# Kernel optimization log

Measured on AMD Instinct MI355X. Metric: run time of the kernel, lower is better.

## Reference

```python
import jax, jax.numpy as jnp
import numpy as np

B, CIN, COUT, SDIM, RES, K = 8, 512, 512, 512, 64, 3
AFF_SCALE = 1.0 / np.sqrt(SDIM)          # LinearAct: 1/sqrt(in_features)
CONV_SCALE = 1.0 / np.sqrt(CIN * K * K)  # ModulatedConv2d: 1/sqrt(in*k*k)
LRELU_GAIN = np.sqrt(2.0)                # bias_act 'lrelu' default gain


def setup_inputs() -> dict:
    key = jax.random.key(0)
    k = jax.random.split(key, 5)
    x = jax.random.normal(k[0], (B, CIN, RES, RES), dtype=jnp.float32)
    w = jax.random.normal(k[1], (B, SDIM), dtype=jnp.float32)
    noise = jax.random.normal(k[2], (B, 1, RES, RES), dtype=jnp.float32)
    affine_w = jax.random.normal(k[3], (CIN, SDIM), dtype=jnp.float32)
    affine_b = jnp.ones((CIN,), dtype=jnp.float32)          # bias.data.fill_(1.0)
    conv_w = jax.random.normal(k[4], (COUT, CIN, K, K), dtype=jnp.float32)
    noise_scale = jnp.asarray(0.1, dtype=jnp.float32)        # InjectNoise.scale (nonzero for a meaningful test)
    bias = jnp.zeros((COUT,), dtype=jnp.float32)
    return {"x": x, "w": w, "noise": noise, "affine_w": affine_w,
            "affine_b": affine_b, "conv_w": conv_w,
            "noise_scale": noise_scale, "bias": bias}


def reference(x, w, noise, affine_w, affine_b, conv_w, noise_scale, bias):
    # affine (LinearAct, act='linear'): style = w @ (W*scale)^T + b
    style = jnp.einsum('bs,cs->bc', w, affine_w * AFF_SCALE) + affine_b  # [B, CIN]

    # modulate + demodulate: per-sample weight [B, COUT, CIN, K, K]
    wt = conv_w[None] * style[:, None, :, None, None] * CONV_SCALE
    d = jax.lax.rsqrt(jnp.sum(wt * wt, axis=(2, 3, 4), keepdims=True) + 1e-8)
    wt = wt * d

    # grouped conv (groups=B) == per-sample conv; flip_weight=True -> plain correlation
    def conv_one(xi, wi):
        return jax.lax.conv_general_dilated(
            xi[None], wi, window_strides=(1, 1), padding=[(1, 1), (1, 1)],
            dimension_numbers=('NCHW', 'OIHW', 'NCHW'))[0]

    y = jax.vmap(conv_one)(x, wt)  # [B, COUT, RES, RES]

    # noise -> bias -> lrelu(0.2) * sqrt(2)
    y = y + noise * noise_scale
    y = jax.nn.leaky_relu(y + bias[None, :, None, None], 0.2) * LRELU_GAIN
    return y
```

## Files before the change

kernel.cpp:

```cpp
#include <hip/hip_runtime.h>
#include <hip/hip_bf16.h>

typedef unsigned short u16;

#define BATCH 8
#define CIN 512
#define COUT 512
#define SDIM 512
#define RES 64
#define PIX (RES * RES)
#define NKT 72

__device__ __constant__ static const float kAffScale  = 0.04419417382415922f;
__device__ __constant__ static const float kConvScale = 0.014731391274719742f;
__device__ __constant__ static const float kGain      = 1.4142135623730951f;

typedef __bf16 bf16x8 __attribute__((ext_vector_type(8)));
typedef float  f32x4  __attribute__((ext_vector_type(4)));

__global__ void style_k(const float* __restrict__ w, const float* __restrict__ aw,
                        const float* __restrict__ ab, float* __restrict__ style,
                        float* __restrict__ zbuf) {
  int tid = blockIdx.x * 256 + threadIdx.x;
  if (blockIdx.x == 0 && threadIdx.x < 64) zbuf[threadIdx.x] = 0.0f;
  int b = tid >> 9, c = tid & 511;
  const float* wp = w + b * SDIM;
  const float* ap = aw + c * SDIM;
  float s = 0.0f;
  for (int k = 0; k < SDIM; ++k) s += wp[k] * ap[k];
  style[tid] = s * kAffScale + ab[c];
}

__global__ void cw2_k(const float* __restrict__ cw, float* __restrict__ cw2) {
  int tid = blockIdx.x * 256 + threadIdx.x;
  const float* p = cw + tid * 9;
  float s = 0.0f;
  #pragma unroll
  for (int t = 0; t < 9; ++t) { float v = p[t]; s += v * v; }
  cw2[tid] = s;
}

__global__ void fac_k(const float* __restrict__ style, const float* __restrict__ cw2,
                      float* __restrict__ fac) {
  int wid  = blockIdx.x * 4 + (threadIdx.x >> 6);
  int lane = threadIdx.x & 63;
  int b = wid >> 9, o = wid & 511;
  const float* st = style + b * CIN;
  const float* c2 = cw2 + o * CIN;
  float s = 0.0f;
  for (int i = lane; i < CIN; i += 64) { float sv = st[i]; s += sv * sv * c2[i]; }
  #pragma unroll
  for (int off = 32; off; off >>= 1) s += __shfl_xor(s, off);
  if (lane == 0) {
    float d = rsqrtf(s * kConvScale * kConvScale + 1e-8f);
    fac[wid] = d * kConvScale;
  }
}

__global__ void wcast_k(const float* __restrict__ cw, u16* __restrict__ wbt) {
  int tid = blockIdx.x * 256 + threadIdx.x;
  int o = tid >> 9, i = tid & 511;
  const float* p = cw + tid * 9;
  #pragma unroll
  for (int t = 0; t < 9; ++t) {
    __hip_bfloat16 h = __float2bfloat16(p[t]);
    wbt[((size_t)(t * 16 + (i >> 5)) * 512 + o) * 32 + (i & 31)] = *(u16*)&h;
  }
}

__global__ void modx_k(const float* __restrict__ x, const float* __restrict__ style,
                       u16* __restrict__ xst) {
  __shared__ float t[64][65];
  int b  = blockIdx.z;
  int it = blockIdx.y * 64;
  int pt = blockIdx.x * 64;
  int tp = threadIdx.x & 63;
  int tr = threadIdx.x >> 6;
  for (int r = tr; r < 64; r += 4) {
    int i = it + r;
    t[r][tp] = x[(b * CIN + i) * PIX + pt + tp] * style[b * CIN + i];
  }
  __syncthreads();
  int i = it + tp;
  size_t base = ((size_t)(b * 16 + (i >> 5)) * PIX) * 32 + (i & 31);
  for (int r = tr; r < 64; r += 4) {
    __hip_bfloat16 h = __float2bfloat16(t[tp][r]);
    xst[base + (size_t)(pt + r) * 32] = *(u16*)&h;
  }
}

__launch_bounds__(512, 2)
__global__ void gemm_k(const u16* __restrict__ wbt, const u16* __restrict__ xst,
                       const float* __restrict__ fac, const float* __restrict__ noise,
                       const float* __restrict__ nscale_p, const float* __restrict__ bias,
                       const float* __restrict__ zbuf, float* __restrict__ y) {
  __shared__ __align__(16) u16 Abuf[2][16384];
  __shared__ __align__(16) u16 Bbuf[2][16384];

  const int tid = threadIdx.x;
  const int bid = blockIdx.x;
  const int swz = (bid & 7) * 32 + (bid >> 3);
  const int mt = swz >> 7;
  const int nt = swz & 127;
  const int b  = nt >> 4;
  const int pimg  = (nt & 15) * 256;
  const int hbase = pimg >> 6;

  const int lane = tid & 63;
  const int wv = tid >> 6;
  const int wm = wv >> 2;
  const int wn = wv & 3;
  const int l15 = lane & 15, l4 = lane >> 4;
  const int slot = (l4 ^ ((l15 >> 1) & 3)) * 8;

  const int sgE = ((tid & 3) ^ ((tid >> 3) & 3)) << 3;
  int aoff[2], boff[2], hr[2], wc[2];
  #pragma unroll
  for (int p = 0; p < 2; ++p) {
    int row = (p * 512 + tid) >> 2;
    aoff[p] = (mt * 256 + row) * 32 + sgE;
    boff[p] = (pimg + row) * 32 + sgE;
    hr[p] = hbase + (row >> 6);
    wc[p] = row & 63;
  }

  auto stA = [&](int ktx, int kh) {
    if (ktx >= NKT) ktx -= NKT;
    const int d = ktx & 1;
    const u16* pan = wbt + ((size_t)((ktx >> 3) * 16 + ((ktx & 7) << 1) + kh) << 14);
    #pragma unroll
    for (int p = 0; p < 2; ++p) {
      const u16* src = pan + aoff[p];
      __builtin_amdgcn_global_load_lds(
          (const __attribute__((address_space(1))) void*)src,
          (__attribute__((address_space(3))) void*)(&Abuf[d][kh * 8192 + (p * 512 + tid) * 8]),
          16, 0, 0);
    }
  };
  auto stB = [&](int ktx, int kh) {
    if (ktx >= NKT) ktx -= NKT;
    const int tap = ktx >> 3;
    const int dy  = tap < 3 ? -1 : (tap < 6 ? 0 : 1);
    const int dx  = (tap - (tap < 3 ? 0 : (tap < 6 ? 3 : 6))) - 1;
    const int d   = ktx & 1;
    const u16* pan = xst + ((size_t)(b * 16 + ((ktx & 7) << 1) + kh) << 17);
    const int shiftE = (dy * 64 + dx) * 32;
    #pragma unroll
    for (int p = 0; p < 2; ++p) {
      int hh = hr[p] + dy, ww = wc[p] + dx;
      const u16* src = ((unsigned)hh < 64u && (unsigned)ww < 64u)
          ? pan + (boff[p] + shiftE) : (const u16*)zbuf;
      __builtin_amdgcn_global_load_lds(
          (const __attribute__((address_space(1))) void*)src,
          (__attribute__((address_space(3))) void*)(&Bbuf[d][kh * 8192 + (p * 512 + tid) * 8]),
          16, 0, 0);
    }
  };

  f32x4 acc[8][4];
  #pragma unroll
  for (int i = 0; i < 8; ++i)
    #pragma unroll
    for (int j = 0; j < 4; ++j) acc[i][j] = (f32x4){0.f, 0.f, 0.f, 0.f};

  stA(0, 0); stB(0, 0); stA(0, 1); stB(0, 1); stA(1, 0); stB(1, 0);
  asm volatile("s_waitcnt vmcnt(8)" ::: "memory");
  __builtin_amdgcn_s_barrier();

#define LDA(mi, kh) (*(const bf16x8*)&Ab[(kh) * 8192 + (wm * 128 + (mi) * 16 + l15) * 32 + slot])
#define LDB(ni, kh) (*(const bf16x8*)&Bb[(kh) * 8192 + (wn * 64 + (ni) * 16 + l15) * 32 + slot])

  for (int kt = 0; kt < NKT; ++kt) {
    const u16* Ab = &Abuf[kt & 1][0];
    const u16* Bb = &Bbuf[kt & 1][0];
    bf16x8 bfr[4], af[4];

    #pragma unroll
    for (int ni = 0; ni < 4; ++ni) bfr[ni] = LDB(ni, 0);
    #pragma unroll
    for (int j = 0; j < 4; ++j) af[j] = LDA(j, 0);
    stA(kt + 1, 1);
    __builtin_amdgcn_s_barrier();
    __builtin_amdgcn_s_setprio(1);
    #pragma unroll
    for (int j = 0; j < 4; ++j)
      #pragma unroll
      for (int ni = 0; ni < 4; ++ni)
        acc[j][ni] = __builtin_amdgcn_mfma_f32_16x16x32_bf16(af[j], bfr[ni], acc[j][ni], 0, 0, 0);
    __builtin_amdgcn_s_setprio(0);
    __builtin_amdgcn_s_barrier();

    #pragma unroll
    for (int j = 0; j < 4; ++j) af[j] = LDA(4 + j, 0);
    stB(kt + 1, 1);
    __builtin_amdgcn_s_barrier();
    __builtin_amdgcn_s_setprio(1);
    #pragma unroll
    for (int j = 0; j < 4; ++j)
      #pragma unroll
      for (int ni = 0; ni < 4; ++ni)
        acc[4 + j][ni] = __builtin_amdgcn_mfma_f32_16x16x32_bf16(af[j], bfr[ni], acc[4 + j][ni], 0, 0, 0);
    __builtin_amdgcn_s_setprio(0);
    asm volatile("s_waitcnt vmcnt(8)" ::: "memory");
    __builtin_amdgcn_s_barrier();

    #pragma unroll
    for (int ni = 0; ni < 4; ++ni) bfr[ni] = LDB(ni, 1);
    #pragma unroll
    for (int j = 0; j < 4; ++j) af[j] = LDA(j, 1);
    stA(kt + 2, 0);
    __builtin_amdgcn_s_barrier();
    __builtin_amdgcn_s_setprio(1);
    #pragma unroll
    for (int j = 0; j < 4; ++j)
      #pragma unroll
      for (int ni = 0; ni < 4; ++ni)
        acc[j][ni] = __builtin_amdgcn_mfma_f32_16x16x32_bf16(af[j], bfr[ni], acc[j][ni], 0, 0, 0);
    __builtin_amdgcn_s_setprio(0);
    __builtin_amdgcn_s_barrier();

    #pragma unroll
    for (int j = 0; j < 4; ++j) af[j] = LDA(4 + j, 1);
    stB(kt + 2, 0);
    __builtin_amdgcn_s_barrier();
    __builtin_amdgcn_s_setprio(1);
    #pragma unroll
    for (int j = 0; j < 4; ++j)
      #pragma unroll
      for (int ni = 0; ni < 4; ++ni)
        acc[4 + j][ni] = __builtin_amdgcn_mfma_f32_16x16x32_bf16(af[j], bfr[ni], acc[4 + j][ni], 0, 0, 0);
    __builtin_amdgcn_s_setprio(0);
    asm volatile("s_waitcnt vmcnt(8)" ::: "memory");
    __builtin_amdgcn_s_barrier();
  }
#undef LDA
#undef LDB

  const float ns = nscale_p[0];
  float nz[4];
  #pragma unroll
  for (int ni = 0; ni < 4; ++ni) {
    int pix = pimg + wn * 64 + ni * 16 + l15;
    nz[ni] = noise[b * PIX + pix] * ns;
  }
  #pragma unroll
  for (int mi = 0; mi < 8; ++mi) {
    int o = mt * 256 + wm * 128 + mi * 16 + l4 * 4;
    f32x4 fv = *(const f32x4*)&fac[b * COUT + o];
    f32x4 bv = *(const f32x4*)&bias[o];
    #pragma unroll
    for (int r = 0; r < 4; ++r) {
      float* yp = y + (size_t)(b * COUT + o + r) * PIX + pimg + wn * 64 + l15;
      #pragma unroll
      for (int ni = 0; ni < 4; ++ni) {
        float v = acc[mi][ni][r] * fv[r] + nz[ni] + bv[r];
        v = (v > 0.0f ? v : 0.2f * v) * kGain;
        yp[ni * 16] = v;
      }
    }
  }
}

extern "C" void kernel_launch(void* const* d_in, const int* in_sizes, int n_in,
                              void* d_out, int out_size, void* d_ws, size_t ws_size,
                              hipStream_t stream) {
  const float* x      = (const float*)d_in[0];
  const float* w      = (const float*)d_in[1];
  const float* noise  = (const float*)d_in[2];
  const float* aff_w  = (const float*)d_in[3];
  const float* aff_b  = (const float*)d_in[4];
  const float* conv_w = (const float*)d_in[5];
  const float* nscale = (const float*)d_in[6];
  const float* bias   = (const float*)d_in[7];
  float* y = (float*)d_out;

  char* ws = (char*)d_ws;
  float* style = (float*)(ws);
  float* fac   = (float*)(ws + 16384);
  float* cw2   = (float*)(ws + 32768);
  float* zbuf  = (float*)(ws + 1081344);
  u16*   wbt   = (u16*)(ws + 1081600);
  u16*   xst   = (u16*)(ws + 5800192);

  style_k<<<16, 256, 0, stream>>>(w, aff_w, aff_b, style, zbuf);
  cw2_k<<<1024, 256, 0, stream>>>(conv_w, cw2);
  fac_k<<<1024, 256, 0, stream>>>(style, cw2, fac);
  wcast_k<<<1024, 256, 0, stream>>>(conv_w, wbt);
  modx_k<<<dim3(64, 8, 8), 256, 0, stream>>>(x, style, xst);
  gemm_k<<<256, 512, 0, stream>>>(wbt, xst, fac, noise, nscale, bias, zbuf, y);
}
```

Measured before the change: 231.6 us.

## Software-pipeline LDS fragment loads one phase ahead of MFMA in conv loop

Restructures the main GEMM loop so LDS reads for the next MFMA phase are issued before the current phase's MFMAs, using separate register sets (af03/af47, bfr0/bfr1) and prefetching the next k-tile's first fragments across the loop boundary. It replaces some barriers with finer lgkmcnt/vmcnt waits and sched_barriers so LDS latency overlaps tensor math. This costs extra VGPRs, which could reduce occupancy, and depends on the wait counts being exactly right for correctness.

Measured after the change: 217.1 us. 6.3% less time.

```diff
diff --git a/kernel.cpp b/kernel.cpp
--- a/kernel.cpp
+++ b/kernel.cpp
@@ -163,78 +163,93 @@
     #pragma unroll
     for (int j = 0; j < 4; ++j) acc[i][j] = (f32x4){0.f, 0.f, 0.f, 0.f};
 
+#define LDAp(base, mi, kh) (*(const bf16x8*)&(base)[(kh) * 8192 + (wm * 128 + (mi) * 16 + l15) * 32 + slot])
+#define LDBp(base, ni, kh) (*(const bf16x8*)&(base)[(kh) * 8192 + (wn * 64 + (ni) * 16 + l15) * 32 + slot])
+
   stA(0, 0); stB(0, 0); stA(0, 1); stB(0, 1); stA(1, 0); stB(1, 0);
   asm volatile("s_waitcnt vmcnt(8)" ::: "memory");
   __builtin_amdgcn_s_barrier();
 
-#define LDA(mi, kh) (*(const bf16x8*)&Ab[(kh) * 8192 + (wm * 128 + (mi) * 16 + l15) * 32 + slot])
-#define LDB(ni, kh) (*(const bf16x8*)&Bb[(kh) * 8192 + (wn * 64 + (ni) * 16 + l15) * 32 + slot])
+  bf16x8 af03[4], af47[4], bfr0[4], bfr1[4];
+  {
+    const u16* Ab = &Abuf[0][0];
+    const u16* Bb = &Bbuf[0][0];
+    #pragma unroll
+    for (int ni = 0; ni < 4; ++ni) bfr0[ni] = LDBp(Bb, ni, 0);
+    #pragma unroll
+    for (int j = 0; j < 4; ++j) af03[j] = LDAp(Ab, j, 0);
+  }
 
   for (int kt = 0; kt < NKT; ++kt) {
-    const u16* Ab = &Abuf[kt & 1][0];
-    const u16* Bb = &Bbuf[kt & 1][0];
-    bf16x8 bfr[4], af[4];
-
-    #pragma unroll
-    for (int ni = 0; ni < 4; ++ni) bfr[ni] = LDB(ni, 0);
-    #pragma unroll
-    for (int j = 0; j < 4; ++j) af[j] = LDA(j, 0);
+    const u16* Ab  = &Abuf[kt & 1][0];
+    const u16* Bb  = &Bbuf[kt & 1][0];
+    const u16* AbN = &Abuf[(kt + 1) & 1][0];
+    const u16* BbN = &Bbuf[(kt + 1) & 1][0];
+
+    #pragma unroll
+    for (int j = 0; j < 4; ++j) af47[j] = LDAp(Ab, 4 + j, 0);
     stA(kt + 1, 1);
+    asm volatile("s_waitcnt lgkmcnt(4)" ::: "memory");
+    __builtin_amdgcn_sched_barrier(0);
+    __builtin_amdgcn_s_setprio(1);
+    #pragma unroll
+    for (int j = 0; j < 4; ++j)
+      #pragma unroll
+      for (int ni = 0; ni < 4; ++ni)
+        acc[j][ni] = __builtin_amdgcn_mfma_f32_16x16x32_bf16(af03[j], bfr0[ni], acc[j][ni], 0, 0, 0);
+    __builtin_amdgcn_s_setprio(0);
+    asm volatile("s_waitcnt vmcnt(6)" ::: "memory");
     __builtin_amdgcn_s_barrier();
+
+    #pragma unroll
+    for (int ni = 0; ni < 4; ++ni) bfr1[ni] = LDBp(Bb, ni, 1);
+    #pragma unroll
+    for (int j = 0; j < 4; ++j) af03[j] = LDAp(Ab, j, 1);
+    stB(kt + 1, 1);
+    asm volatile("s_waitcnt lgkmcnt(8)" ::: "memory");
+    __builtin_amdgcn_sched_barrier(0);
     __builtin_amdgcn_s_setprio(1);
     #pragma unroll
     for (int j = 0; j < 4; ++j)
       #pragma unroll
       for (int ni = 0; ni < 4; ++ni)
-        acc[j][ni] = __builtin_amdgcn_mfma_f32_16x16x32_bf16(af[j], bfr[ni], acc[j][ni], 0, 0, 0);
+        acc[4 + j][ni] = __builtin_amdgcn_mfma_f32_16x16x32_bf16(af47[j], bfr0[ni], acc[4 + j][ni], 0, 0, 0);
     __builtin_amdgcn_s_setprio(0);
     __builtin_amdgcn_s_barrier();
 
     #pragma unroll
-    for (int j = 0; j < 4; ++j) af[j] = LDA(4 + j, 0);
-    stB(kt + 1, 1);
+    for (int j = 0; j < 4; ++j) af47[j] = LDAp(Ab, 4 + j, 1);
+    stA(kt + 2, 0);
+    asm volatile("s_waitcnt lgkmcnt(4)" ::: "memory");
+    __builtin_amdgcn_sched_barrier(0);
+    __builtin_amdgcn_s_setprio(1);
+    #pragma unroll
+    for (int j = 0; j < 4; ++j)
+      #pragma unroll
+      for (int ni = 0; ni < 4; ++ni)
+        acc[j][ni] = __builtin_amdgcn_mfma_f32_16x16x32_bf16(af03[j], bfr1[ni], acc[j][ni], 0, 0, 0);
+    __builtin_amdgcn_s_setprio(0);
+    asm volatile("s_waitcnt vmcnt(6)" ::: "memory");
     __builtin_amdgcn_s_barrier();
+
+    #pragma unroll
+    for (int ni = 0; ni < 4; ++ni) bfr0[ni] = LDBp(BbN, ni, 0);
+    #pragma unroll
+    for (int j = 0; j < 4; ++j) af03[j] = LDAp(AbN, j, 0);
+    stB(kt + 2, 0);
+    asm volatile("s_waitcnt lgkmcnt(8)" ::: "memory");
+    __builtin_amdgcn_sched_barrier(0);
     __builtin_amdgcn_s_setprio(1);
     #pragma unroll
     for (int j = 0; j < 4; ++j)
       #pragma unroll
       for (int ni = 0; ni < 4; ++ni)
-        acc[4 + j][ni] = __builtin_amdgcn_mfma_f32_16x16x32_bf16(af[j], bfr[ni], acc[4 + j][ni], 0, 0, 0);
-    __builtin_amdgcn_s_setprio(0);
-    asm volatile("s_waitcnt vmcnt(8)" ::: "memory");
-    __builtin_amdgcn_s_barrier();
-
-    #pragma unroll
-    for (int ni = 0; ni < 4; ++ni) bfr[ni] = LDB(ni, 1);
-    #pragma unroll
-    for (int j = 0; j < 4; ++j) af[j] = LDA(j, 1);
-    stA(kt + 2, 0);
-    __builtin_amdgcn_s_barrier();
-    __builtin_amdgcn_s_setprio(1);
-    #pragma unroll
-    for (int j = 0; j < 4; ++j)
-      #pragma unroll
-      for (int ni = 0; ni < 4; ++ni)
-        acc[j][ni] = __builtin_amdgcn_mfma_f32_16x16x32_bf16(af[j], bfr[ni], acc[j][ni], 0, 0, 0);
+        acc[4 + j][ni] = __builtin_amdgcn_mfma_f32_16x16x32_bf16(af47[j], bfr1[ni], acc[4 + j][ni], 0, 0, 0);
     __builtin_amdgcn_s_setprio(0);
     __builtin_amdgcn_s_barrier();
-
-    #pragma unroll
-    for (int j = 0; j < 4; ++j) af[j] = LDA(4 + j, 1);
-    stB(kt + 2, 0);
-    __builtin_amdgcn_s_barrier();
-    __builtin_amdgcn_s_setprio(1);
-    #pragma unroll
-    for (int j = 0; j < 4; ++j)
-      #pragma unroll
-      for (int ni = 0; ni < 4; ++ni)
-        acc[4 + j][ni] = __builtin_amdgcn_mfma_f32_16x16x32_bf16(af[j], bfr[ni], acc[4 + j][ni], 0, 0, 0);
-    __builtin_amdgcn_s_setprio(0);
-    asm volatile("s_waitcnt vmcnt(8)" ::: "memory");
-    __builtin_amdgcn_s_barrier();
-  }
-#undef LDA
-#undef LDB
+  }
+#undef LDAp
+#undef LDBp
 
   const float ns = nscale_p[0];
   float nz[4];
```

## Store activations in zero-padded 66x66 panels and unroll GEMM loop by two

Applied to the files above, without the earlier changes.

Activations are now written into per-channel-group panels with a one-pixel zero border (66x66), filled by a new border-zeroing kernel. This removes the per-load bounds checks and the zbuf redirection in the conv GEMM's B-tile loads. The main loop is unrolled by two so LDS buffer indices are compile-time constants, and explicit lgkmcnt waits plus sched_barriers are added before each MFMA block. The cost is an extra small kernel launch and slightly larger workspace, and the explicit waits may limit the compiler's ability to overlap LDS reads with MFMAs.

New measurement: 204.3 us. -11.8%, faster.

```diff
diff --git a/kernel.cpp b/kernel.cpp
--- a/kernel.cpp
+++ b/kernel.cpp
@@ -10,6 +10,8 @@
 #define RES 64
 #define PIX (RES * RES)
 #define NKT 72
+#define PPIX 4356
+#define PANEL_E 139392
 
 __device__ __constant__ static const float kAffScale  = 0.04419417382415922f;
 __device__ __constant__ static const float kConvScale = 0.014731391274719742f;
@@ -19,10 +21,8 @@
 typedef float  f32x4  __attribute__((ext_vector_type(4)));
 
 __global__ void style_k(const float* __restrict__ w, const float* __restrict__ aw,
-                        const float* __restrict__ ab, float* __restrict__ style,
-                        float* __restrict__ zbuf) {
+                        const float* __restrict__ ab, float* __restrict__ style) {
   int tid = blockIdx.x * 256 + threadIdx.x;
-  if (blockIdx.x == 0 && threadIdx.x < 64) zbuf[threadIdx.x] = 0.0f;
   int b = tid >> 9, c = tid & 511;
   const float* wp = w + b * SDIM;
   const float* ap = aw + c * SDIM;
@@ -65,6 +65,18 @@
   for (int t = 0; t < 9; ++t) {
     __hip_bfloat16 h = __float2bfloat16(p[t]);
     wbt[((size_t)(t * 16 + (i >> 5)) * 512 + o) * 32 + (i & 31)] = *(u16*)&h;
+  }
+}
+
+__global__ void bz_k(u16* __restrict__ xst) {
+  int idx = blockIdx.x * 256 + threadIdx.x;
+  if (idx >= 128 * PPIX) return;
+  int pan = idx / PPIX, pix = idx - pan * PPIX;
+  int h = pix / 66, w = pix - h * 66;
+  if (h == 0 || h == 65 || w == 0 || w == 65) {
+    u16* p = xst + (size_t)pan * PANEL_E + (size_t)pix * 32;
+    int4 z = make_int4(0, 0, 0, 0);
+    ((int4*)p)[0] = z; ((int4*)p)[1] = z; ((int4*)p)[2] = z; ((int4*)p)[3] = z;
   }
 }
 
@@ -82,10 +94,11 @@
   }
   __syncthreads();
   int i = it + tp;
-  size_t base = ((size_t)(b * 16 + (i >> 5)) * PIX) * 32 + (i & 31);
+  size_t pbase = (size_t)(b * 16 + (i >> 5)) * PANEL_E + (i & 31);
   for (int r = tr; r < 64; r += 4) {
-    __hip_bfloat16 h = __float2bfloat16(t[tp][r]);
-    xst[base + (size_t)(pt + r) * 32] = *(u16*)&h;
+    int pix = pt + r, h = pix >> 6, w = pix & 63;
+    __hip_bfloat16 hh = __float2bfloat16(t[tp][r]);
+    xst[pbase + (size_t)((h + 1) * 66 + (w + 1)) * 32] = *(u16*)&hh;
   }
 }
 
@@ -93,7 +106,7 @@
 __global__ void gemm_k(const u16* __restrict__ wbt, const u16* __restrict__ xst,
                        const float* __restrict__ fac, const float* __restrict__ noise,
                        const float* __restrict__ nscale_p, const float* __restrict__ bias,
-                       const float* __restrict__ zbuf, float* __restrict__ y) {
+                       float* __restrict__ y) {
   __shared__ __align__(16) u16 Abuf[2][16384];
   __shared__ __align__(16) u16 Bbuf[2][16384];
 
@@ -114,25 +127,22 @@
   const int slot = (l4 ^ ((l15 >> 1) & 3)) * 8;
 
   const int sgE = ((tid & 3) ^ ((tid >> 3) & 3)) << 3;
-  int aoff[2], boff[2], hr[2], wc[2];
+  int aoffE[2], ppB[2];
   #pragma unroll
   for (int p = 0; p < 2; ++p) {
     int row = (p * 512 + tid) >> 2;
-    aoff[p] = (mt * 256 + row) * 32 + sgE;
-    boff[p] = (pimg + row) * 32 + sgE;
-    hr[p] = hbase + (row >> 6);
-    wc[p] = row & 63;
+    aoffE[p] = (mt * 256 + row) * 32 + sgE;
+    ppB[p]   = ((hbase + (row >> 6) + 1) * 66 + (row & 63) + 1) * 32 + sgE;
   }
 
   auto stA = [&](int ktx, int kh) {
     if (ktx >= NKT) ktx -= NKT;
     const int d = ktx & 1;
-    const u16* pan = wbt + ((size_t)((ktx >> 3) * 16 + ((ktx & 7) << 1) + kh) << 14);
+    const u16* pan = wbt + ((size_t)(2 * ktx + kh) << 14);
     #pragma unroll
     for (int p = 0; p < 2; ++p) {
-      const u16* src = pan + aoff[p];
       __builtin_amdgcn_global_load_lds(
-          (const __attribute__((address_space(1))) void*)src,
+          (const __attribute__((address_space(1))) void*)(pan + aoffE[p]),
           (__attribute__((address_space(3))) void*)(&Abuf[d][kh * 8192 + (p * 512 + tid) * 8]),
           16, 0, 0);
     }
@@ -140,18 +150,14 @@
   auto stB = [&](int ktx, int kh) {
     if (ktx >= NKT) ktx -= NKT;
     const int tap = ktx >> 3;
-    const int dy  = tap < 3 ? -1 : (tap < 6 ? 0 : 1);
-    const int dx  = (tap - (tap < 3 ? 0 : (tap < 6 ? 3 : 6))) - 1;
-    const int d   = ktx & 1;
-    const u16* pan = xst + ((size_t)(b * 16 + ((ktx & 7) << 1) + kh) << 17);
-    const int shiftE = (dy * 64 + dx) * 32;
+    const int t3  = (tap >= 6) ? 2 : (tap >= 3 ? 1 : 0);
+    const int shiftE = ((t3 - 1) * 66 + (tap - t3 * 3 - 1)) * 32;
+    const int d = ktx & 1;
+    const u16* pan = xst + (size_t)(b * 16 + ((ktx & 7) << 1) + kh) * PANEL_E + shiftE;
     #pragma unroll
     for (int p = 0; p < 2; ++p) {
-      int hh = hr[p] + dy, ww = wc[p] + dx;
-      const u16* src = ((unsigned)hh < 64u && (unsigned)ww < 64u)
-          ? pan + (boff[p] + shiftE) : (const u16*)zbuf;
       __builtin_amdgcn_global_load_lds(
-          (const __attribute__((address_space(1))) void*)src,
+          (const __attribute__((address_space(1))) void*)(pan + ppB[p]),
           (__attribute__((address_space(3))) void*)(&Bbuf[d][kh * 8192 + (p * 512 + tid) * 8]),
           16, 0, 0);
     }
@@ -167,72 +173,70 @@
   asm volatile("s_waitcnt vmcnt(8)" ::: "memory");
   __builtin_amdgcn_s_barrier();
 
-#define LDA(mi, kh) (*(const bf16x8*)&Ab[(kh) * 8192 + (wm * 128 + (mi) * 16 + l15) * 32 + slot])
-#define LDB(ni, kh) (*(const bf16x8*)&Bb[(kh) * 8192 + (wn * 64 + (ni) * 16 + l15) * 32 + slot])
-
-  for (int kt = 0; kt < NKT; ++kt) {
-    const u16* Ab = &Abuf[kt & 1][0];
-    const u16* Bb = &Bbuf[kt & 1][0];
-    bf16x8 bfr[4], af[4];
-
-    #pragma unroll
-    for (int ni = 0; ni < 4; ++ni) bfr[ni] = LDB(ni, 0);
-    #pragma unroll
-    for (int j = 0; j < 4; ++j) af[j] = LDA(j, 0);
-    stA(kt + 1, 1);
-    __builtin_amdgcn_s_barrier();
-    __builtin_amdgcn_s_setprio(1);
-    #pragma unroll
-    for (int j = 0; j < 4; ++j)
-      #pragma unroll
-      for (int ni = 0; ni < 4; ++ni)
-        acc[j][ni] = __builtin_amdgcn_mfma_f32_16x16x32_bf16(af[j], bfr[ni], acc[j][ni], 0, 0, 0);
-    __builtin_amdgcn_s_setprio(0);
-    __builtin_amdgcn_s_barrier();
-
-    #pragma unroll
-    for (int j = 0; j < 4; ++j) af[j] = LDA(4 + j, 0);
-    stB(kt + 1, 1);
-    __builtin_amdgcn_s_barrier();
-    __builtin_amdgcn_s_setprio(1);
-    #pragma unroll
-    for (int j = 0; j < 4; ++j)
-      #pragma unroll
-      for (int ni = 0; ni < 4; ++ni)
-        acc[4 + j][ni] = __builtin_amdgcn_mfma_f32_16x16x32_bf16(af[j], bfr[ni], acc[4 + j][ni], 0, 0, 0);
-    __builtin_amdgcn_s_setprio(0);
-    asm volatile("s_waitcnt vmcnt(8)" ::: "memory");
-    __builtin_amdgcn_s_barrier();
-
-    #pragma unroll
-    for (int ni = 0; ni < 4; ++ni) bfr[ni] = LDB(ni, 1);
-    #pragma unroll
-    for (int j = 0; j < 4; ++j) af[j] = LDA(j, 1);
-    stA(kt + 2, 0);
-    __builtin_amdgcn_s_barrier();
-    __builtin_amdgcn_s_setprio(1);
-    #pragma unroll
-    for (int j = 0; j < 4; ++j)
-      #pragma unroll
-      for (int ni = 0; ni < 4; ++ni)
-        acc[j][ni] = __builtin_amdgcn_mfma_f32_16x16x32_bf16(af[j], bfr[ni], acc[j][ni], 0, 0, 0);
-    __builtin_amdgcn_s_setprio(0);
-    __builtin_amdgcn_s_barrier();
-
-    #pragma unroll
-    for (int j = 0; j < 4; ++j) af[j] = LDA(4 + j, 1);
-    stB(kt + 2, 0);
-    __builtin_amdgcn_s_barrier();
-    __builtin_amdgcn_s_setprio(1);
-    #pragma unroll
-    for (int j = 0; j < 4; ++j)
-      #pragma unroll
-      for (int ni = 0; ni < 4; ++ni)
-        acc[4 + j][ni] = __builtin_amdgcn_mfma_f32_16x16x32_bf16(af[j], bfr[ni], acc[4 + j][ni], 0, 0, 0);
-    __builtin_amdgcn_s_setprio(0);
-    asm volatile("s_waitcnt vmcnt(8)" ::: "memory");
-    __builtin_amdgcn_s_barrier();
-  }
+#define LDA(D, mi, kh) (*(const bf16x8*)&Abuf[D][(kh) * 8192 + (wm * 128 + (mi) * 16 + l15) * 32 + slot])
+#define LDB(D, ni, kh) (*(const bf16x8*)&Bbuf[D][(kh) * 8192 + (wn * 64 + (ni) * 16 + l15) * 32 + slot])
+
+#define TILE(D, KT) {                                                          \
+    bf16x8 bfr[4], af[4];                                                      \
+                                                       \
+    _Pragma("unroll") for (int ni = 0; ni < 4; ++ni) bfr[ni] = LDB(D, ni, 0);  \
+    _Pragma("unroll") for (int j = 0; j < 4; ++j) af[j] = LDA(D, j, 0);        \
+    stA((KT) + 1, 1);                                                          \
+    __builtin_amdgcn_s_barrier();                                              \
+    asm volatile("s_waitcnt lgkmcnt(0)" ::: "memory");                         \
+    __builtin_amdgcn_sched_barrier(0);                                         \
+    __builtin_amdgcn_s_setprio(1);                                             \
+    _Pragma("unroll") for (int j = 0; j < 4; ++j)                              \
+      _Pragma("unroll") for (int ni = 0; ni < 4; ++ni)                         \
+        acc[j][ni] = __builtin_amdgcn_mfma_f32_16x16x32_bf16(af[j], bfr[ni], acc[j][ni], 0, 0, 0); \
+    __builtin_amdgcn_s_setprio(0);                                             \
+    __builtin_amdgcn_s_barrier();                                              \
+                                                       \
+    _Pragma("unroll") for (int j = 0; j < 4; ++j) af[j] = LDA(D, 4 + j, 0);    \
+    stB((KT) + 1, 1);                                                          \
+    __builtin_amdgcn_s_barrier();                                              \
+    asm volatile("s_waitcnt lgkmcnt(0)" ::: "memory");                         \
+    __builtin_amdgcn_sched_barrier(0);                                         \
+    __builtin_amdgcn_s_setprio(1);                                             \
+    _Pragma("unroll") for (int j = 0; j < 4; ++j)                              \
+      _Pragma("unroll") for (int ni = 0; ni < 4; ++ni)                         \
+        acc[4 + j][ni] = __builtin_amdgcn_mfma_f32_16x16x32_bf16(af[j], bfr[ni], acc[4 + j][ni], 0, 0, 0); \
+    __builtin_amdgcn_s_setprio(0);                                             \
+    asm volatile("s_waitcnt vmcnt(8)" ::: "memory");                           \
+    __builtin_amdgcn_s_barrier();                                              \
+                                                       \
+    _Pragma("unroll") for (int ni = 0; ni < 4; ++ni) bfr[ni] = LDB(D, ni, 1);  \
+    _Pragma("unroll") for (int j = 0; j < 4; ++j) af[j] = LDA(D, j, 1);        \
+    stA((KT) + 2, 0);                                                          \
+    __builtin_amdgcn_s_barrier();                                              \
+    asm volatile("s_waitcnt lgkmcnt(0)" ::: "memory");                         \
+    __builtin_amdgcn_sched_barrier(0);                                         \
+    __builtin_amdgcn_s_setprio(1);                                             \
+    _Pragma("unroll") for (int j = 0; j < 4; ++j)                              \
+      _Pragma("unroll") for (int ni = 0; ni < 4; ++ni)                         \
+        acc[j][ni] = __builtin_amdgcn_mfma_f32_16x16x32_bf16(af[j], bfr[ni], acc[j][ni], 0, 0, 0); \
+    __builtin_amdgcn_s_setprio(0);                                             \
+    __builtin_amdgcn_s_barrier();                                              \
+                                                       \
+    _Pragma("unroll") for (int j = 0; j < 4; ++j) af[j] = LDA(D, 4 + j, 1);    \
+    stB((KT) + 2, 0);                                                          \
+    __builtin_amdgcn_s_barrier();                                              \
+    asm volatile("s_waitcnt lgkmcnt(0)" ::: "memory");                         \
+    __builtin_amdgcn_sched_barrier(0);                                         \
+    __builtin_amdgcn_s_setprio(1);                                             \
+    _Pragma("unroll") for (int j = 0; j < 4; ++j)                              \
+      _Pragma("unroll") for (int ni = 0; ni < 4; ++ni)                         \
+        acc[4 + j][ni] = __builtin_amdgcn_mfma_f32_16x16x32_bf16(af[j], bfr[ni], acc[4 + j][ni], 0, 0, 0); \
+    __builtin_amdgcn_s_setprio(0);                                             \
+    asm volatile("s_waitcnt vmcnt(8)" ::: "memory");                           \
+    __builtin_amdgcn_s_barrier();                                              \
+  }
+
+  for (int kt = 0; kt < NKT; kt += 2) {
+    TILE(0, kt)
+    TILE(1, kt + 1)
+  }
+#undef TILE
 #undef LDA
 #undef LDB
 
@@ -278,14 +282,14 @@
   float* style = (float*)(ws);
   float* fac   = (float*)(ws + 16384);
   float* cw2   = (float*)(ws + 32768);
-  float* zbuf  = (float*)(ws + 1081344);
   u16*   wbt   = (u16*)(ws + 1081600);
   u16*   xst   = (u16*)(ws + 5800192);
 
-  style_k<<<16, 256, 0, stream>>>(w, aff_w, aff_b, style, zbuf);
+  style_k<<<16, 256, 0, stream>>>(w, aff_w, aff_b, style);
   cw2_k<<<1024, 256, 0, stream>>>(conv_w, cw2);
   fac_k<<<1024, 256, 0, stream>>>(style, cw2, fac);
   wcast_k<<<1024, 256, 0, stream>>>(conv_w, wbt);
+  bz_k<<<(128 * PPIX + 255) / 256, 256, 0, stream>>>(xst);
   modx_k<<<dim3(64, 8, 8), 256, 0, stream>>>(x, style, xst);
-  gemm_k<<<256, 512, 0, stream>>>(wbt, xst, fac, noise, nscale, bias, zbuf, y);
-}
+  gemm_k<<<256, 512, 0, stream>>>(wbt, xst, fac, noise, nscale, bias, y);
+}
```
